# Optimization experiments

Hardware: AMD Instinct MI355X
Metric: run time of the kernel (lower is better)

## Reference

```python
import jax, jax.numpy as jnp
import numpy as np

B, C, S = 4, 512, 8192   # batch, channels, seq len
E = 256                  # q_dim // r1 = projected dim
D = 256                  # dilaion: block size; window width = 2*D (D even)


def setup_inputs() -> dict:
    key = jax.random.key(0)
    ks = jax.random.split(key, 6)
    w = 0.05
    return {
        "x1": jax.random.normal(ks[0], (B, C, S), jnp.float32),
        "mask": jnp.ones((B, 1, S), jnp.float32),
        "Wq": jax.random.normal(ks[1], (E, C), jnp.float32) * w,
        "bq": jnp.zeros((E,), jnp.float32),
        "Wk": jax.random.normal(ks[2], (E, C), jnp.float32) * w,
        "bk": jnp.zeros((E,), jnp.float32),
        "Wv": jax.random.normal(ks[3], (E, C), jnp.float32) * w,
        "bv": jnp.zeros((E,), jnp.float32),
        "Wo": jax.random.normal(ks[4], (C, E), jnp.float32) * w,
        "bo": jnp.zeros((C,), jnp.float32),
    }


def _windows(x, nb, d):
    # x: [B, ch, S] -> nb overlapping windows of width 2d (stride d, halo d//2 each side)
    b, ch, _ = x.shape
    xp = jnp.pad(x, ((0, 0), (0, 0), (d // 2, d // 2)))  # [B, ch, S + d]
    lo = xp[:, :, : nb * d].reshape(b, ch, nb, d)
    hi = xp[:, :, d:].reshape(b, ch, nb, d)
    return jnp.concatenate([lo, hi], axis=-1).transpose(0, 2, 1, 3)  # [B, nb, ch, 2d]


def reference(x1, mask, Wq, bq, Wk, bk, Wv, bv, Wo, bo):
    nb = S // D  # S divisible by D -> no tail padding branch
    # 1x1 conv projections
    q = jnp.einsum('ec,bcs->bes', Wq, x1) + bq[None, :, None]
    k = jnp.einsum('ec,bcs->bes', Wk, x1) + bk[None, :, None]
    v = jnp.einsum('ec,bcs->bes', Wv, x1) + bv[None, :, None]

    qw = q.reshape(B, E, nb, D).transpose(0, 2, 1, 3)   # [B, nb, E, D]
    kw = _windows(k, nb, D)                              # [B, nb, E, 2D]
    vw = _windows(v, nb, D)                              # [B, nb, E, 2D]
    pm = mask[:, 0:1, :]                                 # padding mask [B,1,S]
    pmw = _windows(pm, nb, D)                            # [B, nb, 1, 2D]

    W = 2 * D
    # original loop `window_mask[:, :, i:i+D] = 1 for i in range(D)` -> union covers
    # columns [0, 2D-2]; only the last column stays 0 (rows identical)
    win = (jnp.arange(W) < W - 1).astype(jnp.float32)    # [2D]
    fmask = win[None, None, None, :] * pmw               # [B, nb, 1, 2D]

    energy = jnp.einsum('bneq,bnek->bnqk', qw, kw) / np.float32(np.sqrt(E))
    attn = jax.nn.softmax(energy + jnp.log(fmask + 1e-6), axis=-1) * fmask
    out = jnp.einsum('bnek,bnqk->bneq', vw, attn)        # [B, nb, E, D]

    h = jax.nn.gelu(out, approximate=False)
    h = jnp.einsum('oe,bneq->bnoq', Wo, h) + bo[None, None, :, None]  # [B, nb, C, D]
    y = h.transpose(0, 2, 1, 3).reshape(B, C, nb * D)[:, :, :S]
    return y * mask[:, 0:1, :]
```

## Files before the change

### kernel.cpp

```cpp
#include <hip/hip_runtime.h>
#include <hip/hip_bf16.h>

typedef __attribute__((ext_vector_type(8))) short short8;
typedef __attribute__((ext_vector_type(4))) float f32x4;
typedef __attribute__((ext_vector_type(4))) int int4v;

#define DI __device__ __forceinline__

constexpr int Bq = 4, Cc = 512, Ss = 8192, Ee = 256;
constexpr int SP = 8448;
constexpr long XSLAB = 4194304;

DI unsigned short f2bf(float f) {
    unsigned int u = __float_as_uint(f);
    unsigned int r = u + 0x7fffu + ((u >> 16) & 1u);
    return (unsigned short)(r >> 16);
}

union U16x8 { int4v v; unsigned short u[8]; };

DI void gll16(const void* g, void* l) {
    __builtin_amdgcn_global_load_lds(
        (const __attribute__((address_space(1))) unsigned int*)g,
        (__attribute__((address_space(3))) unsigned int*)l, 16, 0, 0);
}

DI unsigned pkbf(float lo, float hi) {
    unsigned r;
    asm("v_cvt_pk_bf16_f32 %0, %1, %2" : "=v"(r) : "v"(lo), "v"(hi));
    return r;
}

DI short8 mk8(unsigned a, unsigned b, unsigned c, unsigned d) {
    int4v v; v[0] = (int)a; v[1] = (int)b; v[2] = (int)c; v[3] = (int)d;
    union { int4v i; short8 s; } U; U.i = v; return U.s;
}

DI f32x4 max4(f32x4 a, f32x4 b) {
    f32x4 r;
    r[0] = fmaxf(a[0], b[0]); r[1] = fmaxf(a[1], b[1]);
    r[2] = fmaxf(a[2], b[2]); r[3] = fmaxf(a[3], b[3]);
    return r;
}

DI float gelu_t(float x) {
    float x2 = x * x;
    float z = x * (0.7978845608f + 0.0356774081f * x2);
    float az = fabsf(z);
    float e = __expf(-2.f * az);
    float th = (1.f - e) / (1.f + e);
    th = (z < 0.f) ? -th : th;
    return 0.5f * x * (1.f + th);
}

DI int SIG(int k)  { return ((k & 4) << 2) | ((k & 24) >> 1) | (k & 3); }
DI int SIG2(int k) { return SIG(SIG(k)); }

__global__ __launch_bounds__(256) void kpre(
    const float* __restrict__ x1,
    const float* __restrict__ Wq, const float* __restrict__ Wk, const float* __restrict__ Wv,
    const float* __restrict__ Wo, unsigned short* __restrict__ Wqkv_b, unsigned short* __restrict__ Wo_b,
    unsigned short* __restrict__ kTp, unsigned short* __restrict__ vp,
    unsigned short* __restrict__ xTo)
{
    int blk = blockIdx.x, t = threadIdx.x;
    if (blk < 4096) {
        int bb = blk >> 10, inner = blk & 1023;
        const float* x1b = x1 + (long)bb * Cc * Ss;
        unsigned short* xT = xTo + (long)bb * XSLAB;
        __shared__ unsigned short tile[64][72];
        int bs = inner & 127, bc = inner >> 7;
        int s0 = bs * 64, c0 = bc * 64;
        int cl = t >> 4, sl = (t & 15) * 4;
        for (int it = 0; it < 4; ++it) {
            int c = cl + it * 16;
            float4 vv = *(const float4*)(x1b + (long)(c0 + c) * Ss + s0 + sl);
            tile[c][sl + 0] = f2bf(vv.x);
            tile[c][sl + 1] = f2bf(vv.y);
            tile[c][sl + 2] = f2bf(vv.z);
            tile[c][sl + 3] = f2bf(vv.w);
        }
        __syncthreads();
        int s_loc = t >> 2, cseg = (t & 3) * 16;
        for (int half = 0; half < 2; ++half) {
            U16x8 u;
            for (int j = 0; j < 8; ++j) u.u[j] = tile[cseg + half * 8 + j][s_loc];
            *(int4v*)(xT + (long)(s0 + s_loc) * Cc + c0 + cseg + half * 8) = u.v;
        }
    } else if (blk < 5632) {
        int i = (blk - 4096) * 256 + t;
        if (i < 768 * 512) {
            int m = i >> 9, c = i & 511;
            const float* src = (m < 256) ? Wq : ((m < 512) ? Wk : Wv);
            Wqkv_b[i] = f2bf(src[(m & 255) * 512 + c]);
        }
        if (i < 512 * 256) {
            int kap = i & 255;
            int src = (i & ~255) | (kap & ~31) | SIG(kap & 31);
            Wo_b[i] = f2bf(Wo[src]);
        }
    } else {
        int i = (blk - 5632) * 256 + t;
        int4v z = {0, 0, 0, 0};
        if (i < 32768) {
            int b = i >> 13, r = i & 8191;
            int side = r >> 12, off = r & 4095;
            *(int4v*)(kTp + (long)b * SP * 256 + (long)(side ? 8320 : 0) * 256 + off * 8) = z;
        } else {
            int j = i - 32768;
            int b = j >> 13, r = j & 8191;
            int row = r >> 5, side = (r >> 4) & 1, sc = r & 15;
            *(int4v*)(vp + ((long)b * 256 + row) * SP + side * 8320 + sc * 8) = z;
        }
    }
}

__global__ __launch_bounds__(256) void kqkv(
    const unsigned short* __restrict__ xT4, const unsigned short* __restrict__ Wqkv,
    const float* __restrict__ bq, const float* __restrict__ bk, const float* __restrict__ bv,
    unsigned short* __restrict__ qT, unsigned short* __restrict__ kTp, unsigned short* __restrict__ vp)
{
    __shared__ int4v As[1024], Bs[1024];
    int b = blockIdx.y;
    const unsigned short* xT = xT4 + (long)b * XSLAB;
    int wg = blockIdx.x;
    int type = wg >> 7, id = wg & 127;
    const unsigned short *A, *Bt; unsigned short* Op;
    long opitch; const float* bias; bool biasRow;
    if (type < 2) {
        int mt = id >> 1, nt = id & 1;
        A  = xT + (long)(mt * 128) * 512;
        Bt = Wqkv + (long)(type * 256 + nt * 128) * 512;
        if (type == 0)
            Op = qT + (long)b * Ss * Ee + (long)(mt * 128) * Ee + nt * 128;
        else
            Op = kTp + (long)b * SP * Ee + (long)(128 + mt * 128) * Ee + nt * 128;
        opitch = Ee;
        bias = (type ? bk : bq) + nt * 128;
        biasRow = false;
    } else {
        int mt = id >> 6, nt = id & 63;
        A  = Wqkv + (long)(512 + mt * 128) * 512;
        Bt = xT + (long)(nt * 128) * 512;
        Op = vp + (long)b * Ee * SP + (long)(mt * 128) * SP + 128 + nt * 128;
        opitch = SP;
        bias = bv + mt * 128;
        biasRow = true;
    }
    int t = threadIdx.x, lane = t & 63, wv = t >> 6;
    int wr = (wv >> 1) * 64, wc = (wv & 1) * 64;

    int soff[4];
    #pragma unroll
    for (int i = 0; i < 4; ++i) {
        int seg = t + 256 * i, row = seg >> 3, cs = seg & 7;
        soff[i] = row * 512 + ((cs ^ (row & 7)) * 8);
    }
    char* adst = (char*)As + wv * 1024;
    char* bdst = (char*)Bs + wv * 1024;

    f32x4 acc[4][4] = {};
    for (int kk = 0; kk < 8; ++kk) {
        #pragma unroll
        for (int i = 0; i < 4; ++i) {
            gll16(A  + soff[i] + kk * 64, adst + i * 4096);
            gll16(Bt + soff[i] + kk * 64, bdst + i * 4096);
        }
        asm volatile("s_waitcnt vmcnt(0)" ::: "memory");
        __syncthreads();
        for (int ks = 0; ks < 2; ++ks) {
            int csk = ks * 4 + (lane >> 4);
            short8 af[4], bfr[4];
            #pragma unroll
            for (int mi = 0; mi < 4; ++mi) {
                int m = wr + mi * 16 + (lane & 15);
                af[mi] = *(const short8*)&As[m * 8 + (csk ^ (m & 7))];
            }
            #pragma unroll
            for (int ni = 0; ni < 4; ++ni) {
                int nn = wc + ni * 16 + (lane & 15);
                bfr[ni] = *(const short8*)&Bs[nn * 8 + (csk ^ (nn & 7))];
            }
            #pragma unroll
            for (int mi = 0; mi < 4; ++mi)
                #pragma unroll
                for (int ni = 0; ni < 4; ++ni)
                    acc[mi][ni] = __builtin_amdgcn_mfma_f32_16x16x32_bf16(af[mi], bfr[ni], acc[mi][ni], 0, 0, 0);
        }
        __syncthreads();
    }
    for (int mi = 0; mi < 4; ++mi)
        for (int ni = 0; ni < 4; ++ni) {
            int mrow = wr + mi * 16 + ((lane >> 4) * 4);
            int ncol = wc + ni * 16 + (lane & 15);
            int nc2 = biasRow ? ((ncol & ~31) | SIG2(ncol & 31)) : ncol;
            for (int r = 0; r < 4; ++r) {
                float bval = biasRow ? bias[mrow + r] : bias[ncol];
                Op[(long)(mrow + r) * opitch + nc2] = f2bf(acc[mi][ni][r] + bval);
            }
        }
}

__global__ __launch_bounds__(512, 2) void kattn(
    const unsigned short* __restrict__ qT, const unsigned short* __restrict__ kTp,
    const unsigned short* __restrict__ vp,  const unsigned short* __restrict__ Wo_b,
    const float* __restrict__ mask, const float* __restrict__ bo,
    float* __restrict__ y)
{
    __shared__ __align__(16) char SH[71680];
    float* fmaskL  = (float*)(SH + 65536);
    float* l2maskL = (float*)(SH + 67584);
    float* boL     = (float*)(SH + 69632);

    int t = threadIdx.x, lane = t & 63, wv = t >> 6;
    int G = lane >> 4, l15 = lane & 15;

    int phys = blockIdx.x;
    int xx = phys & 7, kk2 = phys >> 3;
    int L = ((xx + 8 * (kk2 >> 1)) << 1) | (kk2 & 1);
    int qh = L & 1, n = (L >> 1) & 31, b = L >> 6;
    int sqw = n * 256 + qh * 128 + wv * 16;

    short8 qfrag[8];
    #pragma unroll
    for (int s = 0; s < 8; ++s)
        qfrag[s] = *(const short8*)(qT + ((long)b * Ss + sqw + l15) * 256 + 32 * s + 8 * G);

    {
        int i = t;
        int sw = n * 256 - 128 + i;
        float f = 0.f;
        if (i != 511 && sw >= 0 && sw < Ss) f = mask[(long)b * Ss + sw];
        fmaskL[i] = f;
        l2maskL[i] = __log2f(f + 1e-6f);
    }
    if (t < 128) ((float4*)boL)[t] = ((const float4*)bo)[t];

    const unsigned short* ksrcp[2];
    const unsigned short* vsrcp[2];
    const unsigned short* wsrcp[2];
    #pragma unroll
    for (int i = 0; i < 2; ++i) {
        int krow = wv * 4 + i * 2 + (lane >> 5);
        ksrcp[i] = kTp + ((long)b * SP + n * 256 + krow) * 256 + (((lane & 31) ^ (krow & 7)) * 8);
        int erow = wv * 32 + i * 16 + (lane >> 2);
        vsrcp[i] = vp + ((long)b * 256 + erow) * SP + n * 256 + (((lane & 3) ^ ((lane >> 2) & 3)) * 8);
        int wrow = wv * 4 + i * 2 + (lane >> 5);
        wsrcp[i] = Wo_b + (long)wrow * 256 + (((lane & 31) ^ (wrow & 7)) * 8);
    }

#define STAGE(CH, BUF) {                                                      \
        char* kl = SH + (BUF) * 16384 + wv * 2048;                            \
        char* vl = SH + 32768 + (BUF) * 16384 + wv * 2048;                    \
        _Pragma("unroll")                                                     \
        for (int i = 0; i < 2; ++i) gll16(ksrcp[i] + (long)(CH) * 8192, kl + i * 1024); \
        _Pragma("unroll")                                                     \
        for (int i = 0; i < 2; ++i) gll16(vsrcp[i] + (CH) * 32, vl + i * 1024);          \
    }
#define WSTAGE(ST, BUF) {                                                     \
        char* wl = SH + (BUF) * 16384 + wv * 2048;                            \
        _Pragma("unroll")                                                     \
        for (int i = 0; i < 2; ++i) gll16(wsrcp[i] + (ST) * 8192, wl + i * 1024); \
    }

    STAGE(0, 0)
    STAGE(1, 1)
    asm volatile("s_waitcnt vmcnt(4) lgkmcnt(0)" ::: "memory");
    __builtin_amdgcn_s_barrier();

    float mrun = -1e30f, lrun = 0.f;
    f32x4 oacc[16] = {};

    #pragma unroll 2
    for (int ch = 0; ch < 16; ++ch) {
        const char* KB = SH + (ch & 1) * 16384;
        const char* VB = SH + 32768 + (ch & 1) * 16384;

        f32x4 eacc[2] = {};
        __builtin_amdgcn_s_setprio(1);
        #pragma unroll
        for (int s = 0; s < 8; ++s) {
            short8 kf[2];
            #pragma unroll
            for (int tt = 0; tt < 2; ++tt)
                kf[tt] = *(const short8*)(KB + (16 * tt + l15) * 512 + (((4 * s + G) ^ (l15 & 7)) * 16));
            #pragma unroll
            for (int tt = 0; tt < 2; ++tt)
                eacc[tt] = __builtin_amdgcn_mfma_f32_16x16x32_bf16(kf[tt], qfrag[s], eacc[tt], 0, 0, 0);
        }
        __builtin_amdgcn_s_setprio(0);

        int w0 = ch * 32;
        f32x4 lm[2], fm[2];
        #pragma unroll
        for (int tt = 0; tt < 2; ++tt) {
            lm[tt] = *(const f32x4*)&l2maskL[w0 + 16 * tt + 4 * G];
            fm[tt] = *(const f32x4*)&fmaskL[w0 + 16 * tt + 4 * G];
        }

        f32x4 ev[2];
        #pragma unroll
        for (int tt = 0; tt < 2; ++tt)
            ev[tt] = eacc[tt] * 0.09016844f + lm[tt];
        f32x4 m4 = max4(ev[0], ev[1]);
        float cm = fmaxf(fmaxf(m4[0], m4[1]), fmaxf(m4[2], m4[3]));
        cm = fmaxf(cm, __shfl_xor(cm, 16));
        cm = fmaxf(cm, __shfl_xor(cm, 32));
        if (__any(cm > mrun + 11.5416f)) {
            float mn = fmaxf(mrun, cm);
            float sc = exp2f(mrun - mn);
            mrun = mn; lrun *= sc;
            #pragma unroll
            for (int et = 0; et < 16; ++et) oacc[et] *= sc;
        }

        unsigned pc[4];
        float ssum = 0.f;
        #pragma unroll
        for (int tt = 0; tt < 2; ++tt) {
            f32x4 p;
            p[0] = exp2f(ev[tt][0] - mrun);
            p[1] = exp2f(ev[tt][1] - mrun);
            p[2] = exp2f(ev[tt][2] - mrun);
            p[3] = exp2f(ev[tt][3] - mrun);
            ssum += (p[0] + p[1]) + (p[2] + p[3]);
            f32x4 pf = p * fm[tt];
            pc[2 * tt]     = pkbf(pf[0], pf[1]);
            pc[2 * tt + 1] = pkbf(pf[2], pf[3]);
        }
        ssum += __shfl_xor(ssum, 16);
        ssum += __shfl_xor(ssum, 32);
        lrun += ssum;

        __builtin_amdgcn_s_setprio(1);
        {
            short8 pf = mk8(pc[0], pc[1], pc[2], pc[3]);
            #pragma unroll
            for (int et = 0; et < 16; ++et) {
                short8 vf = *(const short8*)(VB + (16 * et + l15) * 64 + ((G ^ (l15 & 3)) * 16));
                oacc[et] = __builtin_amdgcn_mfma_f32_16x16x32_bf16(vf, pf, oacc[et], 0, 0, 0);
            }
        }
        __builtin_amdgcn_s_setprio(0);

        asm volatile("s_waitcnt lgkmcnt(0)" ::: "memory");
        __builtin_amdgcn_s_barrier();
        if (ch < 14) {
            STAGE(ch + 2, ch & 1)
            asm volatile("s_waitcnt vmcnt(4)" ::: "memory");
        } else if (ch == 14) {
            WSTAGE(0, 0)
            asm volatile("s_waitcnt vmcnt(2)" ::: "memory");
        }
        __builtin_amdgcn_s_barrier();
    }

    float linv = 1.f / lrun;
    unsigned hc[32];
    #pragma unroll
    for (int et = 0; et < 16; ++et) {
        f32x4 xv = oacc[et] * linv;
        hc[2 * et]     = pkbf(gelu_t(xv[0]), gelu_t(xv[1]));
        hc[2 * et + 1] = pkbf(gelu_t(xv[2]), gelu_t(xv[3]));
    }
    float ym = fmaskL[128 + qh * 128 + wv * 16 + l15];

    WSTAGE(1, 1)
    asm volatile("s_waitcnt vmcnt(2)" ::: "memory");
    __builtin_amdgcn_s_barrier();

    #pragma unroll 2
    for (int step = 0; step < 16; ++step) {
        const char* WB = SH + (step & 1) * 16384;
        __builtin_amdgcn_s_setprio(1);
        #pragma unroll
        for (int otl = 0; otl < 2; ++otl) {
            f32x4 pacc = {};
            #pragma unroll
            for (int s = 0; s < 8; ++s) {
                short8 wf = *(const short8*)(WB + (16 * otl + l15) * 512 + (((4 * s + G) ^ (l15 & 7)) * 16));
                short8 hs = mk8(hc[4 * s], hc[4 * s + 1], hc[4 * s + 2], hc[4 * s + 3]);
                pacc = __builtin_amdgcn_mfma_f32_16x16x32_bf16(wf, hs, pacc, 0, 0, 0);
            }
            int o0 = step * 32 + 16 * otl + 4 * G;
            f32x4 bo4 = *(const f32x4*)&boL[o0];
            #pragma unroll
            for (int r = 0; r < 4; ++r)
                y[((long)b * Cc + o0 + r) * Ss + sqw + l15] = (pacc[r] + bo4[r]) * ym;
        }
        __builtin_amdgcn_s_setprio(0);
        asm volatile("s_waitcnt lgkmcnt(0)" ::: "memory");
        __builtin_amdgcn_s_barrier();
        if (step < 14) {
            WSTAGE(step + 2, step & 1)
            asm volatile("s_waitcnt vmcnt(2)" ::: "memory");
        } else if (step == 14) {
            asm volatile("s_waitcnt vmcnt(0)" ::: "memory");
        }
        __builtin_amdgcn_s_barrier();
    }
#undef STAGE
#undef WSTAGE
}

extern "C" void kernel_launch(void* const* d_in, const int* in_sizes, int n_in,
                              void* d_out, int out_size, void* d_ws, size_t ws_size,
                              hipStream_t stream)
{
    const float* x1   = (const float*)d_in[0];
    const float* mask = (const float*)d_in[1];
    const float* Wq   = (const float*)d_in[2];
    const float* bq   = (const float*)d_in[3];
    const float* Wk   = (const float*)d_in[4];
    const float* bk   = (const float*)d_in[5];
    const float* Wv   = (const float*)d_in[6];
    const float* bv   = (const float*)d_in[7];
    const float* Wo   = (const float*)d_in[8];
    const float* bo   = (const float*)d_in[9];
    float* y = (float*)d_out;

    if (ws_size < 52428800u) return;
    char* w = (char*)d_ws;
    unsigned short* Wqkv_b = (unsigned short*)(w);
    unsigned short* Wo_b   = (unsigned short*)(w + 786432);
    unsigned short* qT     = (unsigned short*)(w + 1048576);
    unsigned short* kTp    = (unsigned short*)(w + 17825792);
    unsigned short* vp     = (unsigned short*)(w + 35127296);
    unsigned short* xT4    = (unsigned short*)d_out;

    kpre<<<5888, 256, 0, stream>>>(x1, Wq, Wk, Wv, Wo, Wqkv_b, Wo_b, kTp, vp, xT4);
    kqkv<<<dim3(384, 4), 256, 0, stream>>>(xT4, Wqkv_b, bq, bk, bv, qT, kTp, vp);
    kattn<<<256, 512, 0, stream>>>(qT, kTp, vp, Wo_b, mask, bo, y);
}
```

Measured before the change: 117.6 us.

## Split attention key window across two wave halves and merge softmax states

```diff
diff --git a/kernel.cpp b/kernel.cpp
--- a/kernel.cpp
+++ b/kernel.cpp
@@ -34,13 +34,6 @@
 DI short8 mk8(unsigned a, unsigned b, unsigned c, unsigned d) {
     int4v v; v[0] = (int)a; v[1] = (int)b; v[2] = (int)c; v[3] = (int)d;
     union { int4v i; short8 s; } U; U.i = v; return U.s;
-}
-
-DI f32x4 max4(f32x4 a, f32x4 b) {
-    f32x4 r;
-    r[0] = fmaxf(a[0], b[0]); r[1] = fmaxf(a[1], b[1]);
-    r[2] = fmaxf(a[2], b[2]); r[3] = fmaxf(a[3], b[3]);
-    return r;
 }
 
 DI float gelu_t(float x) {
@@ -214,12 +207,12 @@
 
     int t = threadIdx.x, lane = t & 63, wv = t >> 6;
     int G = lane >> 4, l15 = lane & 15;
+    int wq = wv & 3, half = wv >> 2;
 
     int phys = blockIdx.x;
-    int xx = phys & 7, kk2 = phys >> 3;
-    int L = ((xx + 8 * (kk2 >> 1)) << 1) | (kk2 & 1);
-    int qh = L & 1, n = (L >> 1) & 31, b = L >> 6;
-    int sqw = n * 256 + qh * 128 + wv * 16;
+    int L = (phys & 7) * 64 + (phys >> 3);
+    int qq = L & 3, n = (L >> 2) & 31, b = L >> 7;
+    int sqw = n * 256 + qq * 64 + wq * 16;
 
     short8 qfrag[8];
     #pragma unroll
@@ -237,158 +230,206 @@
     if (t < 128) ((float4*)boL)[t] = ((const float4*)bo)[t];
 
     const unsigned short* ksrcp[2];
-    const unsigned short* vsrcp[2];
+    #pragma unroll
+    for (int i = 0; i < 2; ++i) {
+        int krow = wq * 4 + i * 2 + (lane >> 5);
+        ksrcp[i] = kTp + ((long)b * SP + n * 256 + half * 256 + krow) * 256
+                 + (((lane & 31) ^ (krow & 7)) * 8);
+    }
+    const unsigned short* vsrcp[4];
+    #pragma unroll
+    for (int i = 0; i < 4; ++i) {
+        int erow = wq * 64 + i * 16 + (lane >> 2);
+        vsrcp[i] = vp + ((long)b * 256 + erow) * SP + n * 256 + half * 256
+                 + (((lane & 3) ^ ((lane >> 2) & 3)) * 8);
+    }
     const unsigned short* wsrcp[2];
     #pragma unroll
     for (int i = 0; i < 2; ++i) {
-        int krow = wv * 4 + i * 2 + (lane >> 5);
-        ksrcp[i] = kTp + ((long)b * SP + n * 256 + krow) * 256 + (((lane & 31) ^ (krow & 7)) * 8);
-        int erow = wv * 32 + i * 16 + (lane >> 2);
-        vsrcp[i] = vp + ((long)b * 256 + erow) * SP + n * 256 + (((lane & 3) ^ ((lane >> 2) & 3)) * 8);
-        int wrow = wv * 4 + i * 2 + (lane >> 5);
-        wsrcp[i] = Wo_b + (long)wrow * 256 + (((lane & 31) ^ (wrow & 7)) * 8);
-    }
-
-#define STAGE(CH, BUF) {                                                      \
-        char* kl = SH + (BUF) * 16384 + wv * 2048;                            \
-        char* vl = SH + 32768 + (BUF) * 16384 + wv * 2048;                    \
+        int lr = wv * 4 + i * 2 + (lane >> 5);
+        long grow = (lr < 16) ? lr : (240 + lr);
+        wsrcp[i] = Wo_b + grow * 256 + (((lane & 31) ^ (lr & 7)) * 8);
+    }
+
+#define STAGE_K(C, BUF) {                                                     \
+        char* kl = SH + half * 16384 + (BUF) * 8192 + wq * 2048;              \
         _Pragma("unroll")                                                     \
-        for (int i = 0; i < 2; ++i) gll16(ksrcp[i] + (long)(CH) * 8192, kl + i * 1024); \
+        for (int i = 0; i < 2; ++i) gll16(ksrcp[i] + (long)(C) * 4096, kl + i * 1024); }
+#define STAGE_V(P) {                                                          \
+        char* vl = SH + 32768 + half * 16384 + wq * 4096;                     \
         _Pragma("unroll")                                                     \
-        for (int i = 0; i < 2; ++i) gll16(vsrcp[i] + (CH) * 32, vl + i * 1024);          \
-    }
-#define WSTAGE(ST, BUF) {                                                     \
-        char* wl = SH + (BUF) * 16384 + wv * 2048;                            \
+        for (int i = 0; i < 4; ++i) gll16(vsrcp[i] + (P) * 32, vl + i * 1024); }
+#define WSTAGE(S, BUF) {                                                      \
+        char* wl = SH + 32768 + (BUF) * 16384 + wv * 2048;                    \
         _Pragma("unroll")                                                     \
-        for (int i = 0; i < 2; ++i) gll16(wsrcp[i] + (ST) * 8192, wl + i * 1024); \
-    }
-
-    STAGE(0, 0)
-    STAGE(1, 1)
-    asm volatile("s_waitcnt vmcnt(4) lgkmcnt(0)" ::: "memory");
+        for (int i = 0; i < 2; ++i) gll16(wsrcp[i] + (S) * 4096, wl + i * 1024); }
+
+#define QKC(KB, EACC) {                                                       \
+        __builtin_amdgcn_s_setprio(1);                                        \
+        _Pragma("unroll")                                                     \
+        for (int s_ = 0; s_ < 8; ++s_) {                                      \
+            short8 kf_ = *(const short8*)((KB) + l15 * 512 + (((4 * s_ + G) ^ (l15 & 7)) * 16)); \
+            EACC = __builtin_amdgcn_mfma_f32_16x16x32_bf16(kf_, qfrag[s_], EACC, 0, 0, 0); \
+        }                                                                     \
+        __builtin_amdgcn_s_setprio(0); }
+
+#define SMAX(EACC, C, PC) {                                                   \
+        int w0_ = half * 256 + (C) * 16;                                      \
+        f32x4 lm_ = *(const f32x4*)&l2maskL[w0_ + 4 * G];                     \
+        f32x4 fm_ = *(const f32x4*)&fmaskL[w0_ + 4 * G];                      \
+        f32x4 ev_ = (EACC) * 0.09016844f + lm_;                               \
+        float cm_ = fmaxf(fmaxf(ev_[0], ev_[1]), fmaxf(ev_[2], ev_[3]));      \
+        cm_ = fmaxf(cm_, __shfl_xor(cm_, 16));                                \
+        cm_ = fmaxf(cm_, __shfl_xor(cm_, 32));                                \
+        if (__any(cm_ > mrun + 11.5416f)) {                                   \
+            float mn_ = fmaxf(mrun, cm_); float sc_ = exp2f(mrun - mn_);      \
+            mrun = mn_; lrun *= sc_;                                          \
+            _Pragma("unroll")                                                 \
+            for (int e_ = 0; e_ < 16; ++e_) oacc[e_] *= sc_;                  \
+        }                                                                     \
+        f32x4 p_;                                                             \
+        p_[0] = exp2f(ev_[0] - mrun); p_[1] = exp2f(ev_[1] - mrun);           \
+        p_[2] = exp2f(ev_[2] - mrun); p_[3] = exp2f(ev_[3] - mrun);           \
+        float ss_ = (p_[0] + p_[1]) + (p_[2] + p_[3]);                        \
+        ss_ += __shfl_xor(ss_, 16); ss_ += __shfl_xor(ss_, 32);               \
+        lrun += ss_;                                                          \
+        f32x4 pf_ = p_ * fm_;                                                 \
+        PC[0] = pkbf(pf_[0], pf_[1]); PC[1] = pkbf(pf_[2], pf_[3]); }
+
+    STAGE_K(0, 0)
+    STAGE_K(1, 1)
+    STAGE_V(0)
+    asm volatile("s_waitcnt vmcnt(0) lgkmcnt(0)" ::: "memory");
     __builtin_amdgcn_s_barrier();
 
     float mrun = -1e30f, lrun = 0.f;
     f32x4 oacc[16] = {};
 
-    #pragma unroll 2
-    for (int ch = 0; ch < 16; ++ch) {
-        const char* KB = SH + (ch & 1) * 16384;
-        const char* VB = SH + 32768 + (ch & 1) * 16384;
-
-        f32x4 eacc[2] = {};
-        __builtin_amdgcn_s_setprio(1);
-        #pragma unroll
-        for (int s = 0; s < 8; ++s) {
-            short8 kf[2];
-            #pragma unroll
-            for (int tt = 0; tt < 2; ++tt)
-                kf[tt] = *(const short8*)(KB + (16 * tt + l15) * 512 + (((4 * s + G) ^ (l15 & 7)) * 16));
-            #pragma unroll
-            for (int tt = 0; tt < 2; ++tt)
-                eacc[tt] = __builtin_amdgcn_mfma_f32_16x16x32_bf16(kf[tt], qfrag[s], eacc[tt], 0, 0, 0);
-        }
-        __builtin_amdgcn_s_setprio(0);
-
-        int w0 = ch * 32;
-        f32x4 lm[2], fm[2];
-        #pragma unroll
-        for (int tt = 0; tt < 2; ++tt) {
-            lm[tt] = *(const f32x4*)&l2maskL[w0 + 16 * tt + 4 * G];
-            fm[tt] = *(const f32x4*)&fmaskL[w0 + 16 * tt + 4 * G];
-        }
-
-        f32x4 ev[2];
-        #pragma unroll
-        for (int tt = 0; tt < 2; ++tt)
-            ev[tt] = eacc[tt] * 0.09016844f + lm[tt];
-        f32x4 m4 = max4(ev[0], ev[1]);
-        float cm = fmaxf(fmaxf(m4[0], m4[1]), fmaxf(m4[2], m4[3]));
-        cm = fmaxf(cm, __shfl_xor(cm, 16));
-        cm = fmaxf(cm, __shfl_xor(cm, 32));
-        if (__any(cm > mrun + 11.5416f)) {
-            float mn = fmaxf(mrun, cm);
-            float sc = exp2f(mrun - mn);
-            mrun = mn; lrun *= sc;
-            #pragma unroll
-            for (int et = 0; et < 16; ++et) oacc[et] *= sc;
-        }
-
-        unsigned pc[4];
-        float ssum = 0.f;
-        #pragma unroll
-        for (int tt = 0; tt < 2; ++tt) {
-            f32x4 p;
-            p[0] = exp2f(ev[tt][0] - mrun);
-            p[1] = exp2f(ev[tt][1] - mrun);
-            p[2] = exp2f(ev[tt][2] - mrun);
-            p[3] = exp2f(ev[tt][3] - mrun);
-            ssum += (p[0] + p[1]) + (p[2] + p[3]);
-            f32x4 pf = p * fm[tt];
-            pc[2 * tt]     = pkbf(pf[0], pf[1]);
-            pc[2 * tt + 1] = pkbf(pf[2], pf[3]);
-        }
-        ssum += __shfl_xor(ssum, 16);
-        ssum += __shfl_xor(ssum, 32);
-        lrun += ssum;
-
-        __builtin_amdgcn_s_setprio(1);
+    for (int p = 0; p < 8; ++p) {
+        unsigned pcA[2], pcB[2];
         {
-            short8 pf = mk8(pc[0], pc[1], pc[2], pc[3]);
+            const char* KB = SH + half * 16384;
+            f32x4 eacc = {};
+            QKC(KB, eacc)
+            SMAX(eacc, 2 * p, pcA)
+        }
+        asm volatile("s_waitcnt lgkmcnt(0)" ::: "memory");
+        __builtin_amdgcn_s_barrier();
+        if (p < 7) {
+            STAGE_K(2 * p + 2, 0)
+            asm volatile("s_waitcnt vmcnt(2)" ::: "memory");
+        } else {
+            asm volatile("s_waitcnt vmcnt(0)" ::: "memory");
+        }
+        __builtin_amdgcn_s_barrier();
+        {
+            const char* KB = SH + half * 16384 + 8192;
+            f32x4 eacc = {};
+            QKC(KB, eacc)
+            SMAX(eacc, 2 * p + 1, pcB)
+            const char* VB = SH + 32768 + half * 16384;
+            short8 pf = mk8(pcA[0], pcA[1], pcB[0], pcB[1]);
+            __builtin_amdgcn_s_setprio(1);
             #pragma unroll
             for (int et = 0; et < 16; ++et) {
                 short8 vf = *(const short8*)(VB + (16 * et + l15) * 64 + ((G ^ (l15 & 3)) * 16));
                 oacc[et] = __builtin_amdgcn_mfma_f32_16x16x32_bf16(vf, pf, oacc[et], 0, 0, 0);
             }
-        }
-        __builtin_amdgcn_s_setprio(0);
-
+            __builtin_amdgcn_s_setprio(0);
+        }
         asm volatile("s_waitcnt lgkmcnt(0)" ::: "memory");
         __builtin_amdgcn_s_barrier();
-        if (ch < 14) {
-            STAGE(ch + 2, ch & 1)
-            asm volatile("s_waitcnt vmcnt(4)" ::: "memory");
-        } else if (ch == 14) {
-            WSTAGE(0, 0)
-            asm volatile("s_waitcnt vmcnt(2)" ::: "memory");
-        }
-        __builtin_amdgcn_s_barrier();
-    }
-
-    float linv = 1.f / lrun;
-    unsigned hc[32];
-    #pragma unroll
-    for (int et = 0; et < 16; ++et) {
-        f32x4 xv = oacc[et] * linv;
-        hc[2 * et]     = pkbf(gelu_t(xv[0]), gelu_t(xv[1]));
-        hc[2 * et + 1] = pkbf(gelu_t(xv[2]), gelu_t(xv[3]));
-    }
-    float ym = fmaskL[128 + qh * 128 + wv * 16 + l15];
-
+        if (p < 7) {
+            STAGE_K(2 * p + 3, 1)
+            STAGE_V(p + 1)
+            asm volatile("s_waitcnt vmcnt(6)" ::: "memory");
+        }
+        __builtin_amdgcn_s_barrier();
+    }
+
+    if (wv >= 4) {
+        if (lane < 16) {
+            l2maskL[wq * 32 + l15 * 2]     = mrun;
+            l2maskL[wq * 32 + l15 * 2 + 1] = lrun;
+        }
+        #pragma unroll
+        for (int et = 0; et < 8; ++et)
+            *(f32x4*)(SH + 32768 + wq * 8192 + et * 1024 + lane * 16) = oacc[et];
+    }
+    asm volatile("s_waitcnt lgkmcnt(0)" ::: "memory");
+    __builtin_amdgcn_s_barrier();
+
+    float s1 = 1.f, s2 = 0.f, linv = 0.f;
+    if (wv < 4) {
+        float m2  = l2maskL[wq * 32 + l15 * 2];
+        float l2v = l2maskL[wq * 32 + l15 * 2 + 1];
+        float mm = fmaxf(mrun, m2);
+        s1 = exp2f(mrun - mm);
+        s2 = exp2f(m2 - mm);
+        float ll = lrun * s1 + l2v * s2;
+        linv = 1.f / ll;
+        #pragma unroll
+        for (int et = 0; et < 8; ++et) {
+            f32x4 o2 = *(const f32x4*)(SH + 32768 + wq * 8192 + et * 1024 + lane * 16);
+            oacc[et] = oacc[et] * s1 + o2 * s2;
+        }
+    }
+    asm volatile("s_waitcnt lgkmcnt(0)" ::: "memory");
+    __builtin_amdgcn_s_barrier();
+    if (wv >= 4) {
+        #pragma unroll
+        for (int et = 8; et < 16; ++et)
+            *(f32x4*)(SH + 32768 + wq * 8192 + (et - 8) * 1024 + lane * 16) = oacc[et];
+    }
+    asm volatile("s_waitcnt lgkmcnt(0)" ::: "memory");
+    __builtin_amdgcn_s_barrier();
+    if (wv < 4) {
+        #pragma unroll
+        for (int et = 8; et < 16; ++et) {
+            f32x4 o2 = *(const f32x4*)(SH + 32768 + wq * 8192 + (et - 8) * 1024 + lane * 16);
+            oacc[et] = oacc[et] * s1 + o2 * s2;
+        }
+        #pragma unroll
+        for (int s8 = 0; s8 < 8; ++s8) {
+            f32x4 xa = oacc[2 * s8]     * linv;
+            f32x4 xb = oacc[2 * s8 + 1] * linv;
+            int4v hv;
+            hv[0] = (int)pkbf(gelu_t(xa[0]), gelu_t(xa[1]));
+            hv[1] = (int)pkbf(gelu_t(xa[2]), gelu_t(xa[3]));
+            hv[2] = (int)pkbf(gelu_t(xb[0]), gelu_t(xb[1]));
+            hv[3] = (int)pkbf(gelu_t(xb[2]), gelu_t(xb[3]));
+            *(int4v*)(SH + wq * 8192 + s8 * 1024 + lane * 16) = hv;
+        }
+    }
+    asm volatile("s_waitcnt lgkmcnt(0)" ::: "memory");
+    __builtin_amdgcn_s_barrier();
+
+    short8 hs[8];
+    #pragma unroll
+    for (int s8 = 0; s8 < 8; ++s8)
+        hs[s8] = *(const short8*)(SH + wq * 8192 + s8 * 1024 + lane * 16);
+    float ym = fmaskL[128 + qq * 64 + wq * 16 + l15];
+
+    WSTAGE(0, 0)
     WSTAGE(1, 1)
     asm volatile("s_waitcnt vmcnt(2)" ::: "memory");
     __builtin_amdgcn_s_barrier();
 
-    #pragma unroll 2
     for (int step = 0; step < 16; ++step) {
-        const char* WB = SH + (step & 1) * 16384;
+        const char* WB = SH + 32768 + (step & 1) * 16384;
+        f32x4 pacc = {};
         __builtin_amdgcn_s_setprio(1);
         #pragma unroll
-        for (int otl = 0; otl < 2; ++otl) {
-            f32x4 pacc = {};
-            #pragma unroll
-            for (int s = 0; s < 8; ++s) {
-                short8 wf = *(const short8*)(WB + (16 * otl + l15) * 512 + (((4 * s + G) ^ (l15 & 7)) * 16));
-                short8 hs = mk8(hc[4 * s], hc[4 * s + 1], hc[4 * s + 2], hc[4 * s + 3]);
-                pacc = __builtin_amdgcn_mfma_f32_16x16x32_bf16(wf, hs, pacc, 0, 0, 0);
-            }
-            int o0 = step * 32 + 16 * otl + 4 * G;
-            f32x4 bo4 = *(const f32x4*)&boL[o0];
-            #pragma unroll
-            for (int r = 0; r < 4; ++r)
-                y[((long)b * Cc + o0 + r) * Ss + sqw + l15] = (pacc[r] + bo4[r]) * ym;
+        for (int s8 = 0; s8 < 8; ++s8) {
+            short8 wf = *(const short8*)(WB + (half * 16 + l15) * 512 + (((4 * s8 + G) ^ (l15 & 7)) * 16));
+            pacc = __builtin_amdgcn_mfma_f32_16x16x32_bf16(wf, hs[s8], pacc, 0, 0, 0);
         }
         __builtin_amdgcn_s_setprio(0);
+        int o0 = half * 256 + 16 * step + 4 * G;
+        f32x4 bo4 = *(const f32x4*)&boL[o0];
+        #pragma unroll
+        for (int r = 0; r < 4; ++r)
+            y[((long)b * Cc + o0 + r) * Ss + sqw + l15] = (pacc[r] + bo4[r]) * ym;
         asm volatile("s_waitcnt lgkmcnt(0)" ::: "memory");
         __builtin_amdgcn_s_barrier();
         if (step < 14) {
@@ -399,8 +440,11 @@
         }
         __builtin_amdgcn_s_barrier();
     }
-#undef STAGE
+#undef STAGE_K
+#undef STAGE_V
 #undef WSTAGE
+#undef QKC
+#undef SMAX
 }
 
 extern "C" void kernel_launch(void* const* d_in, const int* in_sizes, int n_in,
@@ -430,5 +474,5 @@
 
     kpre<<<5888, 256, 0, stream>>>(x1, Wq, Wk, Wv, Wo, Wqkv_b, Wo_b, kTp, vp, xT4);
     kqkv<<<dim3(384, 4), 256, 0, stream>>>(xT4, Wqkv_b, bq, bk, bv, qT, kTp, vp);
-    kattn<<<256, 512, 0, stream>>>(qT, kTp, vp, Wo_b, mask, bo, y);
-}
+    kattn<<<512, 512, 0, stream>>>(qT, kTp, vp, Wo_b, mask, bo, y);
+}
```

After: 134.5 us. +14.4%, slower.
